# Optimization experiments

Measured on AMD Instinct MI355X. Metric: run time of the kernel, lower is better.

Reference implementation:

```python
import jax, jax.numpy as jnp
import numpy as np

N_NODES = 100000
N_FEAT = 512
HIDDEN = 64
N_CLASS = 40
N_EDGES = 3200000


def setup_inputs() -> dict:
    key = jax.random.key(0)
    k1, k2, k3, k4, k5, k6 = jax.random.split(key, 6)
    x = jax.random.normal(k1, (N_NODES, N_FEAT), dtype=jnp.float32)
    edge_index = jax.random.randint(k2, (2, N_EDGES), 0, N_NODES, dtype=jnp.int64)
    # Glorot-style init like PyG GCNConv
    s1 = (6.0 / (N_FEAT + HIDDEN)) ** 0.5
    s2 = (6.0 / (HIDDEN + N_CLASS)) ** 0.5
    W1 = jax.random.uniform(k3, (N_FEAT, HIDDEN), jnp.float32, -s1, s1)
    b1 = jnp.zeros((HIDDEN,), jnp.float32)
    W2 = jax.random.uniform(k4, (HIDDEN, N_CLASS), jnp.float32, -s2, s2)
    b2 = jnp.zeros((N_CLASS,), jnp.float32)
    return {"x": x, "edge_index": edge_index, "W1": W1, "b1": b1, "W2": W2, "b2": b2}


def _gcn_norm(edge_index, n_nodes):
    # add self-loops, symmetric normalization (PyG gcn_norm defaults)
    loops = jnp.arange(n_nodes, dtype=edge_index.dtype)
    src = jnp.concatenate([edge_index[0], loops])
    dst = jnp.concatenate([edge_index[1], loops])
    deg = jax.ops.segment_sum(jnp.ones_like(dst, dtype=jnp.float32), dst,
                              num_segments=n_nodes)
    dinv = jnp.where(deg > 0, jax.lax.rsqrt(deg), 0.0)
    norm = dinv[src] * dinv[dst]  # [E + N]
    return src, dst, norm


def _gcn_conv(h, src, dst, norm, W, b, n_nodes):
    h = h @ W                                   # [N, out]
    msg = h[src] * norm[:, None]                # gather + scale, [E+N, out]
    out = jax.ops.segment_sum(msg, dst, num_segments=n_nodes)  # scatter-add
    return out + b


def reference(x, edge_index, W1, b1, W2, b2):
    n = x.shape[0]
    src, dst, norm = _gcn_norm(edge_index, n)
    h = _gcn_conv(x, src, dst, norm, W1, b1, n)
    h = jax.nn.relu(h)
    h = _gcn_conv(h, src, dst, norm, W2, b2, n)
    return jax.nn.softmax(h, axis=-1)
```

## Files before the change

kernel.cpp:

```cpp
#include <hip/hip_runtime.h>
#include <hip/hip_bf16.h>
#include <math.h>

#define NFEAT 512
#define HID   64
#define NCLS  40

#define BSHIFT 9
#define BSIZE  512
#define BCAP   20480
#define CHUNK  4096

struct __align__(8) bf16x4 { __hip_bfloat16 a, b, c, d; };

__device__ __forceinline__ float rl_f(float v, int l) {
    return __int_as_float(__builtin_amdgcn_readlane(__float_as_int(v), l));
}


__global__ __launch_bounds__(256) void bin_scatter(const int* __restrict__ ei, int e,
                                                   int nbuckets,
                                                   int* __restrict__ bucket_cursor,
                                                   int* __restrict__ stage) {
    __shared__ int packed_s[CHUNK];
    __shared__ unsigned char bkt_s[CHUNK];
    __shared__ int hist[256];
    __shared__ int base_s[256];
    __shared__ int lcur[256];
    int t = threadIdx.x;
    int b0 = blockIdx.x * CHUNK;
    int cnt = min(CHUNK, e - b0);
    for (int i = t; i < 256; i += 256) hist[i] = 0;
    __syncthreads();
    for (int i = t; i < cnt; i += 256) {
        int s = ei[b0 + i];
        int d = ei[e + b0 + i];
        packed_s[i] = (s << BSHIFT) | (d & (BSIZE - 1));
        bkt_s[i] = (unsigned char)(d >> BSHIFT);
        atomicAdd(&hist[d >> BSHIFT], 1);
    }
    __syncthreads();
    for (int i = t; i < nbuckets; i += 256) {
        int c = hist[i];
        base_s[i] = c ? atomicAdd(&bucket_cursor[i], c) : 0;
        lcur[i] = 0;
    }
    __syncthreads();
    for (int i = t; i < cnt; i += 256) {
        int bk = bkt_s[i];
        int pos = base_s[bk] + atomicAdd(&lcur[bk], 1);
        if (pos < BCAP) stage[(size_t)bk * BCAP + pos] = packed_s[i];
    }
}

__global__ __launch_bounds__(256) void bucket_scan(const int* __restrict__ bucket_cursor,
                                                   int* __restrict__ bucket_base,
                                                   int nbuckets, int n, int e,
                                                   int* __restrict__ row_ptr) {
    __shared__ int sc[256];
    int t = threadIdx.x;
    int v = (t < nbuckets) ? bucket_cursor[t] : 0;
    sc[t] = v;
    __syncthreads();
    #pragma unroll
    for (int off = 1; off < 256; off <<= 1) {
        int u = (t >= off) ? sc[t - off] : 0;
        __syncthreads();
        sc[t] += u;
        __syncthreads();
    }
    if (t < nbuckets) bucket_base[t] = sc[t] - v;
    if (t == 0) row_ptr[n] = e;
}

__global__ __launch_bounds__(256) void bucket_csr(const int* __restrict__ stage,
                                                  const int* __restrict__ bucket_cursor,
                                                  const int* __restrict__ bucket_base,
                                                  int* __restrict__ row_ptr,
                                                  float* __restrict__ dinv,
                                                  int* __restrict__ col, int n) {
    __shared__ int hist[BSIZE];
    __shared__ int lbase[BSIZE];
    __shared__ int psum[256];
    int b = blockIdx.x;
    int t = threadIdx.x;
    int cnt = min(bucket_cursor[b], BCAP);
    int node0 = b << BSHIFT;
    int nnodes = min(BSIZE, n - node0);
    const int* st = stage + (size_t)b * BCAP;
    for (int i = t; i < BSIZE; i += 256) hist[i] = 0;
    __syncthreads();
    for (int i = t; i < cnt; i += 256) atomicAdd(&hist[st[i] & (BSIZE - 1)], 1);
    __syncthreads();
    int h0 = hist[2 * t], h1 = hist[2 * t + 1];
    int pair = h0 + h1;
    psum[t] = pair;
    __syncthreads();
    #pragma unroll
    for (int off = 1; off < 256; off <<= 1) {
        int u = (t >= off) ? psum[t - off] : 0;
        __syncthreads();
        psum[t] += u;
        __syncthreads();
    }
    int ex = psum[t] - pair;
    lbase[2 * t] = ex;
    lbase[2 * t + 1] = ex + h0;
    __syncthreads();
    int base0 = bucket_base[b];
    for (int i = t; i < nnodes; i += 256) {
        row_ptr[node0 + i] = base0 + lbase[i];
        dinv[node0 + i] = rsqrtf((float)(hist[i] + 1));
    }
    __syncthreads();
    for (int i = t; i < cnt; i += 256) {
        int p = st[i];
        int pos = atomicAdd(&lbase[p & (BSIZE - 1)], 1);
        col[base0 + pos] = ((unsigned)p) >> BSHIFT;
    }
}


__global__ __launch_bounds__(256) void gemm1(const float* __restrict__ x,
                                             const float* __restrict__ W1,
                                             const float* __restrict__ dinv,
                                             __hip_bfloat16* __restrict__ t1, int n) {
    __shared__ __align__(16) float xst[32][68];
    __shared__ __align__(16) float wsh[32][64];
    int m0 = blockIdx.x * 64;
    int t = threadIdx.x;
    int tr = t >> 4;
    int tc = t & 15;
    float acc[4][4] = {};

    for (int k0 = 0; k0 < NFEAT; k0 += 32) {
        #pragma unroll
        for (int s = 0; s < 2; s++) {
            int slot = t + s * 256;
            int row = slot >> 3;
            int kv  = slot & 7;
            int grow = m0 + row;
            if (grow >= n) grow = n - 1;
            float4 v = *(const float4*)(x + (size_t)grow * NFEAT + k0 + kv * 4);
            xst[kv * 4 + 0][row] = v.x;
            xst[kv * 4 + 1][row] = v.y;
            xst[kv * 4 + 2][row] = v.z;
            xst[kv * 4 + 3][row] = v.w;
        }
        #pragma unroll
        for (int s = 0; s < 2; s++) {
            int slot = t + s * 256;
            int kr = slot >> 4;
            int cv = slot & 15;
            float4 v = *(const float4*)(W1 + (size_t)(k0 + kr) * HID + cv * 4);
            *(float4*)(&wsh[kr][cv * 4]) = v;
        }
        __syncthreads();
        #pragma unroll
        for (int k = 0; k < 32; k++) {
            float4 a = *(const float4*)(&xst[k][tr * 4]);
            float4 b = *(const float4*)(&wsh[k][tc * 4]);
            acc[0][0] += a.x * b.x; acc[0][1] += a.x * b.y; acc[0][2] += a.x * b.z; acc[0][3] += a.x * b.w;
            acc[1][0] += a.y * b.x; acc[1][1] += a.y * b.y; acc[1][2] += a.y * b.z; acc[1][3] += a.y * b.w;
            acc[2][0] += a.z * b.x; acc[2][1] += a.z * b.y; acc[2][2] += a.z * b.z; acc[2][3] += a.z * b.w;
            acc[3][0] += a.w * b.x; acc[3][1] += a.w * b.y; acc[3][2] += a.w * b.z; acc[3][3] += a.w * b.w;
        }
        __syncthreads();
    }
    #pragma unroll
    for (int i = 0; i < 4; i++) {
        int row = m0 + tr * 4 + i;
        if (row < n) {
            float d = dinv[row];
            bf16x4 o;
            o.a = __float2bfloat16(acc[i][0] * d);
            o.b = __float2bfloat16(acc[i][1] * d);
            o.c = __float2bfloat16(acc[i][2] * d);
            o.d = __float2bfloat16(acc[i][3] * d);
            *(bf16x4*)(t1 + (size_t)row * HID + tc * 4) = o;
        }
    }
}


#define UNPACK_ADD(pv) do { \
    acc[0] += __uint_as_float((pv).x << 16); acc[1] += __uint_as_float((pv).x & 0xffff0000u); \
    acc[2] += __uint_as_float((pv).y << 16); acc[3] += __uint_as_float((pv).y & 0xffff0000u); \
    acc[4] += __uint_as_float((pv).z << 16); acc[5] += __uint_as_float((pv).z & 0xffff0000u); \
    acc[6] += __uint_as_float((pv).w << 16); acc[7] += __uint_as_float((pv).w & 0xffff0000u); } while (0)

__global__ __launch_bounds__(256) void agg1_gemm2(const __hip_bfloat16* __restrict__ t1,
                                                  const int* __restrict__ row_ptr,
                                                  const int* __restrict__ col,
                                                  const float* __restrict__ dinv,
                                                  const float* __restrict__ b1,
                                                  const float* __restrict__ W2,
                                                  __hip_bfloat16* __restrict__ t2, int n) {
    __shared__ float2 w2p[32 * 40];
    for (int i = threadIdx.x; i < 32 * 40; i += 256) {
        int k2 = i / 40, c = i - k2 * 40;
        w2p[i] = make_float2(W2[(2 * k2) * 40 + c], W2[(2 * k2 + 1) * 40 + c]);
    }
    __syncthreads();

    int wave = threadIdx.x >> 6;
    int lane = threadIdx.x & 63;
    int node0 = blockIdx.x * 4 + wave;
    int node = (node0 < n) ? node0 : n - 1;
    int r = lane & 7;
    int slot = lane >> 3;

    const uint4* t1q = (const uint4*)t1;
    int s0 = row_ptr[node], s1 = row_ptr[node + 1];

    float acc[8] = {0.f, 0.f, 0.f, 0.f, 0.f, 0.f, 0.f, 0.f};

    if (lane < 8) {
        uint4 pv = t1q[(size_t)node * 8 + lane];
        UNPACK_ADD(pv);
    }

    int bpbase = slot * 4;
    for (int jb = s0; jb < s1; jb += 32) {
        int rem = s1 - jb;
        int ll = lane & 31;
        int cidx = col[jb + ((ll < rem) ? ll : 0)];
        int srcg[4];
        #pragma unroll
        for (int g = 0; g < 4; g++) {
            int src = __builtin_amdgcn_ds_bpermute(bpbase + 32 * g, cidx);
            srcg[g] = (8 * g + slot < rem) ? src : n;
        }
        uint4 pv[4];
        #pragma unroll
        for (int g = 0; g < 4; g++) pv[g] = t1q[(size_t)srcg[g] * 8 + r];
        #pragma unroll
        for (int g = 0; g < 4; g++) { UNPACK_ADD(pv[g]); }
    }

    #pragma unroll
    for (int off = 8; off < 64; off <<= 1) {
        #pragma unroll
        for (int j = 0; j < 8; j++) acc[j] += __shfl_xor(acc[j], off, 64);
    }

    float dn = dinv[node];
    const float4* b1q = (const float4*)b1;
    float4 ba = b1q[2 * r];
    float4 bb = b1q[2 * r + 1];
    float hv[8];
    hv[0] = fmaxf(0.f, dn * acc[0] + ba.x);
    hv[1] = fmaxf(0.f, dn * acc[1] + ba.y);
    hv[2] = fmaxf(0.f, dn * acc[2] + ba.z);
    hv[3] = fmaxf(0.f, dn * acc[3] + ba.w);
    hv[4] = fmaxf(0.f, dn * acc[4] + bb.x);
    hv[5] = fmaxf(0.f, dn * acc[5] + bb.y);
    hv[6] = fmaxf(0.f, dn * acc[6] + bb.z);
    hv[7] = fmaxf(0.f, dn * acc[7] + bb.w);

    int c = (lane < 40) ? lane : 39;
    float o = 0.0f;
    #pragma unroll
    for (int rr = 0; rr < 8; rr++) {
        #pragma unroll
        for (int j2 = 0; j2 < 4; j2++) {
            float ha = rl_f(hv[2 * j2],     rr);
            float hb = rl_f(hv[2 * j2 + 1], rr);
            float2 w = w2p[(4 * rr + j2) * 40 + c];
            o += ha * w.x + hb * w.y;
        }
    }
    if (node0 < n && lane < 40) t2[(size_t)node * NCLS + lane] = __float2bfloat16(dn * o);
}


__global__ __launch_bounds__(256) void agg2_softmax(const __hip_bfloat16* __restrict__ t2,
                                                    const int* __restrict__ row_ptr,
                                                    const int* __restrict__ col,
                                                    const float* __restrict__ dinv,
                                                    const float* __restrict__ b2,
                                                    float* __restrict__ out, int n) {
    int wave = threadIdx.x >> 6;
    int lane = threadIdx.x & 63;
    int node = blockIdx.x * 4 + wave;
    if (node >= n) return;
    int h = lane >> 5;
    int p = lane & 31;
    int pc = (p < 20) ? p : 19;
    const unsigned* t2d = (const unsigned*)t2;
    int s0 = row_ptr[node], s1 = row_ptr[node + 1];

    float ax = 0.f, ay = 0.f;
    if (h == 0) {
        unsigned v = t2d[(size_t)node * 20 + pc];
        ax = __uint_as_float(v << 16);
        ay = __uint_as_float(v & 0xffff0000u);
    }
    for (int jb = s0; jb < s1; jb += 16) {
        int rem = s1 - jb;
        int cv = col[jb + ((lane < rem) ? lane : 0)];
        int srcg[8];
        #pragma unroll
        for (int i = 0; i < 8; i++) {
            int eid = 2 * i + h;
            int src = __builtin_amdgcn_ds_bpermute(4 * eid, cv);
            srcg[i] = (eid < rem) ? src : n;
        }
        unsigned pv[8];
        #pragma unroll
        for (int i = 0; i < 8; i++) pv[i] = t2d[(size_t)srcg[i] * 20 + pc];
        #pragma unroll
        for (int i = 0; i < 8; i++) {
            ax += __uint_as_float(pv[i] << 16);
            ay += __uint_as_float(pv[i] & 0xffff0000u);
        }
    }
    ax += __shfl_xor(ax, 32, 64);
    ay += __shfl_xor(ay, 32, 64);

    float dn = dinv[node];
    float2 bv = *(const float2*)(b2 + 2 * pc);
    float lx = dn * ax + bv.x;
    float ly = dn * ay + bv.y;
    float m = (p < 20) ? fmaxf(lx, ly) : -INFINITY;
    #pragma unroll
    for (int off = 16; off; off >>= 1) m = fmaxf(m, __shfl_xor(m, off, 64));
    float ex = (p < 20) ? expf(lx - m) : 0.0f;
    float ey = (p < 20) ? expf(ly - m) : 0.0f;
    float ssum = ex + ey;
    #pragma unroll
    for (int off = 16; off; off >>= 1) ssum += __shfl_xor(ssum, off, 64);
    if (h == 0 && p < 20) {
        *(float2*)(out + (size_t)node * NCLS + 2 * p) = make_float2(ex / ssum, ey / ssum);
    }
}


static inline size_t align256(size_t x) { return (x + 255) & ~(size_t)255; }

extern "C" void kernel_launch(void* const* d_in, const int* in_sizes, int n_in,
                              void* d_out, int out_size, void* d_ws, size_t ws_size,
                              hipStream_t stream) {
    const float* x  = (const float*)d_in[0];
    const int*   ei = (const int*)d_in[1];
    const float* W1 = (const float*)d_in[2];
    const float* b1 = (const float*)d_in[3];
    const float* W2 = (const float*)d_in[4];
    const float* b2 = (const float*)d_in[5];
    float* out = (float*)d_out;

    const int n = in_sizes[0] / NFEAT;
    const int e = in_sizes[1] / 2;
    const int nbuckets = (n + BSIZE - 1) >> BSHIFT;

    char* ws = (char*)d_ws;
    size_t off = 0;
    int*   row_ptr  = (int*)(ws + off);   off += align256((size_t)(n + 1) * 4);
    float* dinv     = (float*)(ws + off); off += align256((size_t)n * 4);
    int*   bcursor  = (int*)(ws + off);   off += align256(256 * 4);
    int*   bbase    = (int*)(ws + off);   off += align256(256 * 4);
    int*   col      = (int*)(ws + off);   off += align256((size_t)e * 4);
    int*   stage    = (int*)(ws + off);   off += align256((size_t)nbuckets * BCAP * 4);
    __hip_bfloat16* t1 = (__hip_bfloat16*)(ws + off); off += align256((size_t)(n + 1) * HID * 2);
    __hip_bfloat16* t2 = (__hip_bfloat16*)(ws + off); off += align256((size_t)(n + 1) * NCLS * 2);

    (void)hipMemsetAsync(bcursor, 0, 256 * 4, stream);
    (void)hipMemsetAsync(t1 + (size_t)n * HID, 0, HID * 2, stream);
    (void)hipMemsetAsync(t2 + (size_t)n * NCLS, 0, NCLS * 2, stream);
    bin_scatter<<<(e + CHUNK - 1) / CHUNK, 256, 0, stream>>>(ei, e, nbuckets, bcursor, stage);
    bucket_scan<<<1, 256, 0, stream>>>(bcursor, bbase, nbuckets, n, e, row_ptr);
    bucket_csr<<<nbuckets, 256, 0, stream>>>(stage, bcursor, bbase, row_ptr, dinv, col, n);
    gemm1<<<(n + 63) / 64, 256, 0, stream>>>(x, W1, dinv, t1, n);
    agg1_gemm2<<<(n + 3) / 4, 256, 0, stream>>>(t1, row_ptr, col, dinv, b1, W2, t2, n);
    agg2_softmax<<<(n + 3) / 4, 256, 0, stream>>>(t2, row_ptr, col, dinv, b2, out, n);
}
```

Measured before the change: 562.5 us.

## Use bf16 MFMA for gemm1, fold bucket scan into csr, pad t2 rows

gemm1 is rewritten to convert x tiles to bf16 and run them through 16x16x32 bf16 MFMA instructions, replacing the fp32 FMA outer-product loop. W1 is pre-transposed to bf16 by a small new kernel. The separate single-block bucket_scan launch is removed: each bucket_csr block now recomputes the prefix scan over bucket counts itself. The t2 row stride is padded from 40 to 64 bf16 values for aligned gathers, which adds memory footprint and reduces the precision of the first matmul inputs.

Result: faster. 550.8 us (-2.1%).

```diff
diff --git a/kernel.cpp b/kernel.cpp
--- a/kernel.cpp
+++ b/kernel.cpp
@@ -5,16 +5,22 @@
 #define NFEAT 512
 #define HID   64
 #define NCLS  40
+#define T2STRIDE 64
 
 #define BSHIFT 9
 #define BSIZE  512
 #define BCAP   20480
 #define CHUNK  4096
 
-struct __align__(8) bf16x4 { __hip_bfloat16 a, b, c, d; };
+typedef __attribute__((ext_vector_type(8))) short bf16x8v;
+typedef __attribute__((ext_vector_type(4))) float f32x4v;
 
 __device__ __forceinline__ float rl_f(float v, int l) {
     return __int_as_float(__builtin_amdgcn_readlane(__float_as_int(v), l));
+}
+__device__ __forceinline__ unsigned short f2bf(float f) {
+    __hip_bfloat16 h = __float2bfloat16(f);
+    return *(unsigned short*)&h;
 }
 
 
@@ -53,37 +59,31 @@
     }
 }
 
-__global__ __launch_bounds__(256) void bucket_scan(const int* __restrict__ bucket_cursor,
-                                                   int* __restrict__ bucket_base,
-                                                   int nbuckets, int n, int e,
-                                                   int* __restrict__ row_ptr) {
-    __shared__ int sc[256];
-    int t = threadIdx.x;
-    int v = (t < nbuckets) ? bucket_cursor[t] : 0;
-    sc[t] = v;
-    __syncthreads();
-    #pragma unroll
-    for (int off = 1; off < 256; off <<= 1) {
-        int u = (t >= off) ? sc[t - off] : 0;
-        __syncthreads();
-        sc[t] += u;
-        __syncthreads();
-    }
-    if (t < nbuckets) bucket_base[t] = sc[t] - v;
-    if (t == 0) row_ptr[n] = e;
-}
-
 __global__ __launch_bounds__(256) void bucket_csr(const int* __restrict__ stage,
                                                   const int* __restrict__ bucket_cursor,
-                                                  const int* __restrict__ bucket_base,
                                                   int* __restrict__ row_ptr,
                                                   float* __restrict__ dinv,
-                                                  int* __restrict__ col, int n) {
+                                                  int* __restrict__ col,
+                                                  int n, int e, int nbuckets) {
+    __shared__ int sc[256];
     __shared__ int hist[BSIZE];
     __shared__ int lbase[BSIZE];
     __shared__ int psum[256];
     int b = blockIdx.x;
     int t = threadIdx.x;
+    int v = (t < nbuckets) ? bucket_cursor[t] : 0;
+    sc[t] = v;
+    __syncthreads();
+    #pragma unroll
+    for (int off = 1; off < 256; off <<= 1) {
+        int u = (t >= off) ? sc[t - off] : 0;
+        __syncthreads();
+        sc[t] += u;
+        __syncthreads();
+    }
+    int base0 = (b > 0) ? sc[b - 1] : 0;
+    if (b == 0 && t == 0) row_ptr[n] = e;
+
     int cnt = min(bucket_cursor[b], BCAP);
     int node0 = b << BSHIFT;
     int nnodes = min(BSIZE, n - node0);
@@ -107,7 +107,6 @@
     lbase[2 * t] = ex;
     lbase[2 * t + 1] = ex + h0;
     __syncthreads();
-    int base0 = bucket_base[b];
     for (int i = t; i < nnodes; i += 256) {
         row_ptr[node0 + i] = base0 + lbase[i];
         dinv[node0 + i] = rsqrtf((float)(hist[i] + 1));
@@ -121,63 +120,57 @@
 }
 
 
+__global__ __launch_bounds__(256) void w1_to_bf16t(const float* __restrict__ W1,
+                                                   unsigned short* __restrict__ w1bt) {
+    int idx = blockIdx.x * 256 + threadIdx.x;
+    int c = idx >> 9, k = idx & 511;
+    w1bt[idx] = f2bf(W1[k * HID + c]);
+}
+
+
 __global__ __launch_bounds__(256) void gemm1(const float* __restrict__ x,
-                                             const float* __restrict__ W1,
+                                             const unsigned short* __restrict__ w1bt,
                                              const float* __restrict__ dinv,
                                              __hip_bfloat16* __restrict__ t1, int n) {
-    __shared__ __align__(16) float xst[32][68];
-    __shared__ __align__(16) float wsh[32][64];
+    __shared__ __align__(16) unsigned short As[64][40];
+    __shared__ __align__(16) unsigned short Bs[64][40];
+    int t = threadIdx.x;
     int m0 = blockIdx.x * 64;
-    int t = threadIdx.x;
-    int tr = t >> 4;
-    int tc = t & 15;
-    float acc[4][4] = {};
+    int w = t >> 6, lane = t & 63;
+    int lrow = lane & 15, lkg = lane >> 4;
+    f32x4v acc[4] = {};
+
+    int arow = t >> 2;
+    int akg = t & 3;
+    int grow = m0 + arow; if (grow >= n) grow = n - 1;
+    const float* xrow = x + (size_t)grow * NFEAT;
 
     for (int k0 = 0; k0 < NFEAT; k0 += 32) {
-        #pragma unroll
-        for (int s = 0; s < 2; s++) {
-            int slot = t + s * 256;
-            int row = slot >> 3;
-            int kv  = slot & 7;
-            int grow = m0 + row;
-            if (grow >= n) grow = n - 1;
-            float4 v = *(const float4*)(x + (size_t)grow * NFEAT + k0 + kv * 4);
-            xst[kv * 4 + 0][row] = v.x;
-            xst[kv * 4 + 1][row] = v.y;
-            xst[kv * 4 + 2][row] = v.z;
-            xst[kv * 4 + 3][row] = v.w;
-        }
-        #pragma unroll
-        for (int s = 0; s < 2; s++) {
-            int slot = t + s * 256;
-            int kr = slot >> 4;
-            int cv = slot & 15;
-            float4 v = *(const float4*)(W1 + (size_t)(k0 + kr) * HID + cv * 4);
-            *(float4*)(&wsh[kr][cv * 4]) = v;
-        }
-        __syncthreads();
-        #pragma unroll
-        for (int k = 0; k < 32; k++) {
-            float4 a = *(const float4*)(&xst[k][tr * 4]);
-            float4 b = *(const float4*)(&wsh[k][tc * 4]);
-            acc[0][0] += a.x * b.x; acc[0][1] += a.x * b.y; acc[0][2] += a.x * b.z; acc[0][3] += a.x * b.w;
-            acc[1][0] += a.y * b.x; acc[1][1] += a.y * b.y; acc[1][2] += a.y * b.z; acc[1][3] += a.y * b.w;
-            acc[2][0] += a.z * b.x; acc[2][1] += a.z * b.y; acc[2][2] += a.z * b.z; acc[2][3] += a.z * b.w;
-            acc[3][0] += a.w * b.x; acc[3][1] += a.w * b.y; acc[3][2] += a.w * b.z; acc[3][3] += a.w * b.w;
-        }
-        __syncthreads();
-    }
-    #pragma unroll
-    for (int i = 0; i < 4; i++) {
-        int row = m0 + tr * 4 + i;
+        float4 v0 = *(const float4*)(xrow + k0 + akg * 8);
+        float4 v1 = *(const float4*)(xrow + k0 + akg * 8 + 4);
+        union { unsigned short u[8]; uint4 q; } P;
+        P.u[0] = f2bf(v0.x); P.u[1] = f2bf(v0.y); P.u[2] = f2bf(v0.z); P.u[3] = f2bf(v0.w);
+        P.u[4] = f2bf(v1.x); P.u[5] = f2bf(v1.y); P.u[6] = f2bf(v1.z); P.u[7] = f2bf(v1.w);
+        *(uint4*)&As[arow][akg * 8] = P.q;
+        *(uint4*)&Bs[arow][akg * 8] = *(const uint4*)(w1bt + arow * 512 + k0 + akg * 8);
+        __syncthreads();
+        bf16x8v af = *(const bf16x8v*)&As[w * 16 + lrow][lkg * 8];
+        #pragma unroll
+        for (int nb = 0; nb < 4; nb++) {
+            bf16x8v bfv = *(const bf16x8v*)&Bs[nb * 16 + lrow][lkg * 8];
+            acc[nb] = __builtin_amdgcn_mfma_f32_16x16x32_bf16(af, bfv, acc[nb], 0, 0, 0);
+        }
+        __syncthreads();
+    }
+    #pragma unroll
+    for (int r = 0; r < 4; r++) {
+        int row = m0 + w * 16 + lkg * 4 + r;
         if (row < n) {
             float d = dinv[row];
-            bf16x4 o;
-            o.a = __float2bfloat16(acc[i][0] * d);
-            o.b = __float2bfloat16(acc[i][1] * d);
-            o.c = __float2bfloat16(acc[i][2] * d);
-            o.d = __float2bfloat16(acc[i][3] * d);
-            *(bf16x4*)(t1 + (size_t)row * HID + tc * 4) = o;
+            #pragma unroll
+            for (int nb = 0; nb < 4; nb++) {
+                t1[(size_t)row * HID + nb * 16 + lrow] = __float2bfloat16(acc[nb][r] * d);
+            }
         }
     }
 }
@@ -266,11 +259,12 @@
         for (int j2 = 0; j2 < 4; j2++) {
             float ha = rl_f(hv[2 * j2],     rr);
             float hb = rl_f(hv[2 * j2 + 1], rr);
-            float2 w = w2p[(4 * rr + j2) * 40 + c];
-            o += ha * w.x + hb * w.y;
-        }
-    }
-    if (node0 < n && lane < 40) t2[(size_t)node * NCLS + lane] = __float2bfloat16(dn * o);
+            float2 wv = w2p[(4 * rr + j2) * 40 + c];
+            o += ha * wv.x + hb * wv.y;
+        }
+    }
+    if (node0 < n && lane < 40)
+        t2[(size_t)node * T2STRIDE + lane] = __float2bfloat16(dn * o);
 }
 
 
@@ -292,7 +286,7 @@
 
     float ax = 0.f, ay = 0.f;
     if (h == 0) {
-        unsigned v = t2d[(size_t)node * 20 + pc];
+        unsigned v = t2d[(size_t)node * 32 + pc];
         ax = __uint_as_float(v << 16);
         ay = __uint_as_float(v & 0xffff0000u);
     }
@@ -308,7 +302,7 @@
         }
         unsigned pv[8];
         #pragma unroll
-        for (int i = 0; i < 8; i++) pv[i] = t2d[(size_t)srcg[i] * 20 + pc];
+        for (int i = 0; i < 8; i++) pv[i] = t2d[(size_t)srcg[i] * 32 + pc];
         #pragma unroll
         for (int i = 0; i < 8; i++) {
             ax += __uint_as_float(pv[i] << 16);
@@ -358,19 +352,19 @@
     int*   row_ptr  = (int*)(ws + off);   off += align256((size_t)(n + 1) * 4);
     float* dinv     = (float*)(ws + off); off += align256((size_t)n * 4);
     int*   bcursor  = (int*)(ws + off);   off += align256(256 * 4);
-    int*   bbase    = (int*)(ws + off);   off += align256(256 * 4);
     int*   col      = (int*)(ws + off);   off += align256((size_t)e * 4);
     int*   stage    = (int*)(ws + off);   off += align256((size_t)nbuckets * BCAP * 4);
+    unsigned short* w1bt = (unsigned short*)(ws + off); off += align256((size_t)HID * NFEAT * 2);
     __hip_bfloat16* t1 = (__hip_bfloat16*)(ws + off); off += align256((size_t)(n + 1) * HID * 2);
-    __hip_bfloat16* t2 = (__hip_bfloat16*)(ws + off); off += align256((size_t)(n + 1) * NCLS * 2);
+    __hip_bfloat16* t2 = (__hip_bfloat16*)(ws + off); off += align256((size_t)(n + 1) * T2STRIDE * 2);
 
     (void)hipMemsetAsync(bcursor, 0, 256 * 4, stream);
     (void)hipMemsetAsync(t1 + (size_t)n * HID, 0, HID * 2, stream);
-    (void)hipMemsetAsync(t2 + (size_t)n * NCLS, 0, NCLS * 2, stream);
+    (void)hipMemsetAsync(t2 + (size_t)n * T2STRIDE, 0, T2STRIDE * 2, stream);
+    w1_to_bf16t<<<(HID * NFEAT) / 256, 256, 0, stream>>>(W1, w1bt);
     bin_scatter<<<(e + CHUNK - 1) / CHUNK, 256, 0, stream>>>(ei, e, nbuckets, bcursor, stage);
-    bucket_scan<<<1, 256, 0, stream>>>(bcursor, bbase, nbuckets, n, e, row_ptr);
-    bucket_csr<<<nbuckets, 256, 0, stream>>>(stage, bcursor, bbase, row_ptr, dinv, col, n);
-    gemm1<<<(n + 63) / 64, 256, 0, stream>>>(x, W1, dinv, t1, n);
+    bucket_csr<<<nbuckets, 256, 0, stream>>>(stage, bcursor, row_ptr, dinv, col, n, e, nbuckets);
+    gemm1<<<(n + 63) / 64, 256, 0, stream>>>(x, w1bt, dinv, t1, n);
     agg1_gemm2<<<(n + 3) / 4, 256, 0, stream>>>(t1, row_ptr, col, dinv, b1, W2, t2, n);
     agg2_softmax<<<(n + 3) / 4, 256, 0, stream>>>(t2, row_ptr, col, dinv, b2, out, n);
 }
```
